# Kernel tuning notes

Hardware: AMD Instinct MI355X
Metric: run time of the kernel (lower is better)

The kernel has to match this reference:

```python
import jax, jax.numpy as jnp
import numpy as np

M, B, T, DIN, H, E, NEMB = 6, 128, 32, 64, 512, 512, 32


def setup_inputs() -> dict:
    key = jax.random.key(0)
    ks = jax.random.split(key, 6)
    return {
        "state_btD": jax.random.normal(ks[0], (B, T, M * DIN), dtype=jnp.float32),
        "emb_ids": jax.random.randint(ks[1], (B,), 0, NEMB),
        # stacked per-modality, per-embodiment adapter params (all modalities share dims)
        "W1": 0.02 * jax.random.normal(ks[2], (M, NEMB, DIN, H), dtype=jnp.float32),
        "b1": jnp.zeros((M, NEMB, H), dtype=jnp.float32),
        "W2": 0.02 * jax.random.normal(ks[3], (M, NEMB, H, E), dtype=jnp.float32),
        "b2": jnp.zeros((M, NEMB, E), dtype=jnp.float32),
        "type_embed": 0.02 * jax.random.normal(ks[4], (M, E), dtype=jnp.float32),
    }


def reference(state_btD, emb_ids, W1, b1, W2, b2, type_embed):
    Bb, Tt, _ = state_btD.shape
    # slices are contiguous equal-size chunks -> (B, T, M, DIN)
    x = state_btD.reshape(Bb, Tt, M, DIN)
    # layer1: per-sample gathered weights W1[:, emb_ids] -> (M, B, DIN, H)
    h = jax.nn.relu(
        jnp.einsum('btmi,mbih->btmh', x, W1[:, emb_ids])
        + b1[:, emb_ids].transpose(1, 0, 2)[:, None]  # (B,1,M,H)
    )
    # layer2 + type embed
    z = (
        jnp.einsum('btmh,mbho->btmo', h, W2[:, emb_ids])
        + b2[:, emb_ids].transpose(1, 0, 2)[:, None]
        + type_embed[None, None]  # (1,1,M,E)
    )
    # torch.cat(tokens, dim=1): modality-major along the token axis -> (B, M*T, E)
    return z.transpose(0, 2, 1, 3).reshape(Bb, M * Tt, E)
```

## Files before the change

kernel.cpp:

```cpp
#include <hip/hip_runtime.h>

#define MM   6
#define BB   128
#define TT   32
#define DIN  64
#define HH   512
#define EE   512
#define NEMB 32
#define XP   72
#define HP   520

typedef __attribute__((ext_vector_type(8))) short bf16x8;
typedef __attribute__((ext_vector_type(4))) float f32x4;

static __device__ __forceinline__ unsigned short f2bf(float f) {
    unsigned int u = __float_as_uint(f);
    u += 0x7FFFu + ((u >> 16) & 1u);
    return (unsigned short)(u >> 16);
}
static __device__ __forceinline__ float bf2f(unsigned short h) {
    return __uint_as_float(((unsigned int)h) << 16);
}
static __device__ __forceinline__ unsigned short f2bf_t(float f) {
    return (unsigned short)(__float_as_uint(f) >> 16);
}

__global__ void order_k(const int* __restrict__ emb_ids, int* __restrict__ ent) {
    __shared__ int cnt_s[NEMB], psum_s[NEMB], slot_s[BB], id_s[BB];
    int t = threadIdx.x;
    if (t < NEMB) cnt_s[t] = 0;
    __syncthreads();
    if (t < BB) { int id = emb_ids[t]; id_s[t] = id; slot_s[t] = atomicAdd(&cnt_s[id], 1); }
    __syncthreads();
    if (t == 0) { int r = 0; for (int i = 0; i < NEMB; ++i) { psum_s[i] = r; r += cnt_s[i]; } }
    __syncthreads();
    if (t < BB) {
        int id = id_s[t], sl = slot_s[t], base = psum_s[id] * MM, c = cnt_s[id];
        for (int mm = 0; mm < MM; ++mm) ent[base + mm * c + sl] = (t << 3) | mm;
    }
}

__global__ __launch_bounds__(512, 4) void tok_mfma5(
    const float* __restrict__ state,
    const int*   __restrict__ ent,
    const float* __restrict__ W1,
    const float* __restrict__ b1,
    const float* __restrict__ W2,
    const float* __restrict__ b2,
    const float* __restrict__ te,
    const int*   __restrict__ emb_ids,
    float* __restrict__ out)
{
    __shared__ __align__(16) unsigned short x_hi[TT][XP];
    __shared__ __align__(16) unsigned short x_lo[TT][XP];
    __shared__ __align__(16) unsigned short h_hi[TT][HP];
    __shared__ __align__(16) unsigned short h_lo[TT][HP];

    const int bid = blockIdx.x;
    const int s   = (bid & 7) * 96 + (bid >> 3);
    const int e   = ent[s];
    const int b   = e >> 3;
    const int m   = e & 7;
    const int id  = emb_ids[b];

    const int tid  = threadIdx.x;
    const int lane = tid & 63;
    const int w    = tid >> 6;
    const int lr   = lane & 15;
    const int lg   = lane >> 4;

    const float* W1p = W1 + (size_t)(m * NEMB + id) * DIN * HH;
    const float* b1p = b1 + (size_t)(m * NEMB + id) * HH;
    const float* W2p = W2 + (size_t)(m * NEMB + id) * HH * EE;
    const float* b2p = b2 + (size_t)(m * NEMB + id) * EE;
    const float* tep = te + m * EE;
    const float* xg  = state + (size_t)b * TT * (MM * DIN) + m * DIN;

    {
        int t  = tid >> 4;
        int i4 = tid & 15;
        float4 v = *reinterpret_cast<const float4*>(xg + (size_t)t * (MM * DIN) + i4 * 4);
        ushort4 hi, lo;
        hi.x = f2bf(v.x); lo.x = f2bf_t(v.x - bf2f(hi.x));
        hi.y = f2bf(v.y); lo.y = f2bf_t(v.y - bf2f(hi.y));
        hi.z = f2bf(v.z); lo.z = f2bf_t(v.z - bf2f(hi.z));
        hi.w = f2bf(v.w); lo.w = f2bf_t(v.w - bf2f(hi.w));
        *reinterpret_cast<ushort4*>(&x_hi[t][i4 * 4]) = hi;
        *reinterpret_cast<ushort4*>(&x_lo[t][i4 * 4]) = lo;
    }
    __syncthreads();

    bf16x8 xa_h[2][2], xa_l[2][2];
    #pragma unroll
    for (int rt = 0; rt < 2; ++rt)
        #pragma unroll
        for (int kk = 0; kk < 2; ++kk) {
            xa_h[rt][kk] = *reinterpret_cast<const bf16x8*>(&x_hi[rt * 16 + lr][kk * 32 + lg * 8]);
            xa_l[rt][kk] = *reinterpret_cast<const bf16x8*>(&x_lo[rt * 16 + lr][kk * 32 + lg * 8]);
        }

    #pragma unroll
    for (int j = 0; j < 4; ++j) {
        const int n = w * 64 + j * 16 + lr;
        float bv = b1p[n];
        f32x4 a0 = {bv, bv, bv, bv};
        f32x4 a1 = {bv, bv, bv, bv};
        #pragma unroll
        for (int kk = 0; kk < 2; ++kk) {
            const float* wp = W1p + (size_t)(kk * 32 + lg * 8) * HH + n;
            bf16x8 bh, bl;
            #pragma unroll
            for (int i = 0; i < 8; ++i) {
                float wv = wp[(size_t)i * HH];
                unsigned short h_ = f2bf(wv);
                bh[i] = (short)h_;
                bl[i] = (short)f2bf_t(wv - bf2f(h_));
            }
            a0 = __builtin_amdgcn_mfma_f32_16x16x32_bf16(xa_h[0][kk], bh, a0, 0, 0, 0);
            a0 = __builtin_amdgcn_mfma_f32_16x16x32_bf16(xa_h[0][kk], bl, a0, 0, 0, 0);
            a0 = __builtin_amdgcn_mfma_f32_16x16x32_bf16(xa_l[0][kk], bh, a0, 0, 0, 0);
            a1 = __builtin_amdgcn_mfma_f32_16x16x32_bf16(xa_h[1][kk], bh, a1, 0, 0, 0);
            a1 = __builtin_amdgcn_mfma_f32_16x16x32_bf16(xa_h[1][kk], bl, a1, 0, 0, 0);
            a1 = __builtin_amdgcn_mfma_f32_16x16x32_bf16(xa_l[1][kk], bh, a1, 0, 0, 0);
        }
        #pragma unroll
        for (int r = 0; r < 4; ++r) {
            float h0 = fmaxf(a0[r], 0.0f);
            unsigned short hh0 = f2bf(h0);
            h_hi[lg * 4 + r][n] = hh0;
            h_lo[lg * 4 + r][n] = f2bf_t(h0 - bf2f(hh0));
            float h1 = fmaxf(a1[r], 0.0f);
            unsigned short hh1 = f2bf(h1);
            h_hi[16 + lg * 4 + r][n] = hh1;
            h_lo[16 + lg * 4 + r][n] = f2bf_t(h1 - bf2f(hh1));
        }
    }
    __syncthreads();

    float bias2[4];
    #pragma unroll
    for (int j = 0; j < 4; ++j) {
        int n = w * 64 + j * 16 + lr;
        bias2[j] = b2p[n] + tep[n];
    }
    f32x4 acc[2][4];
    #pragma unroll
    for (int rt = 0; rt < 2; ++rt)
        #pragma unroll
        for (int j = 0; j < 4; ++j) {
            f32x4 t0 = {bias2[j], bias2[j], bias2[j], bias2[j]};
            acc[rt][j] = t0;
        }

    float cur[8];
    #pragma unroll
    for (int i = 0; i < 8; ++i)
        cur[i] = W2p[(size_t)(lg * 8 + i) * EE + (w * 64 + lr)];

    for (int kk = 0; kk < 16; ++kk) {
        bf16x8 ah0 = *reinterpret_cast<const bf16x8*>(&h_hi[lr][kk * 32 + lg * 8]);
        bf16x8 al0 = *reinterpret_cast<const bf16x8*>(&h_lo[lr][kk * 32 + lg * 8]);
        bf16x8 ah1 = *reinterpret_cast<const bf16x8*>(&h_hi[16 + lr][kk * 32 + lg * 8]);
        bf16x8 al1 = *reinterpret_cast<const bf16x8*>(&h_lo[16 + lr][kk * 32 + lg * 8]);
        #pragma unroll
        for (int j = 0; j < 4; ++j) {
            int nkk = (j == 3) ? kk + 1 : kk;
            int nj  = (j == 3) ? 0 : j + 1;
            float nxt[8];
            if (nkk < 16) {
                const float* wp = W2p + (size_t)(nkk * 32 + lg * 8) * EE + (w * 64 + nj * 16 + lr);
                #pragma unroll
                for (int i = 0; i < 8; ++i) nxt[i] = wp[(size_t)i * EE];
            } else {
                #pragma unroll
                for (int i = 0; i < 8; ++i) nxt[i] = 0.0f;
            }
            bf16x8 bh, bl;
            #pragma unroll
            for (int i = 0; i < 8; ++i) {
                unsigned short hb = f2bf(cur[i]);
                bh[i] = (short)hb;
                bl[i] = (short)f2bf_t(cur[i] - bf2f(hb));
            }
            acc[0][j] = __builtin_amdgcn_mfma_f32_16x16x32_bf16(ah0, bh, acc[0][j], 0, 0, 0);
            acc[0][j] = __builtin_amdgcn_mfma_f32_16x16x32_bf16(ah0, bl, acc[0][j], 0, 0, 0);
            acc[0][j] = __builtin_amdgcn_mfma_f32_16x16x32_bf16(al0, bh, acc[0][j], 0, 0, 0);
            acc[1][j] = __builtin_amdgcn_mfma_f32_16x16x32_bf16(ah1, bh, acc[1][j], 0, 0, 0);
            acc[1][j] = __builtin_amdgcn_mfma_f32_16x16x32_bf16(ah1, bl, acc[1][j], 0, 0, 0);
            acc[1][j] = __builtin_amdgcn_mfma_f32_16x16x32_bf16(al1, bh, acc[1][j], 0, 0, 0);
            #pragma unroll
            for (int i = 0; i < 8; ++i) cur[i] = nxt[i];
        }
    }

    float* outp = out + ((size_t)(b * MM + m) * TT) * EE;
    #pragma unroll
    for (int rt = 0; rt < 2; ++rt)
        #pragma unroll
        for (int j = 0; j < 4; ++j) {
            int n = w * 64 + j * 16 + lr;
            #pragma unroll
            for (int r = 0; r < 4; ++r) {
                int row = rt * 16 + lg * 4 + r;
                outp[(size_t)row * EE + n] = acc[rt][j][r];
            }
        }
}

extern "C" void kernel_launch(void* const* d_in, const int* in_sizes, int n_in,
                              void* d_out, int out_size, void* d_ws, size_t ws_size,
                              hipStream_t stream) {
    const float* state   = (const float*)d_in[0];
    const int*   emb_ids = (const int*)d_in[1];
    const float* W1      = (const float*)d_in[2];
    const float* b1      = (const float*)d_in[3];
    const float* W2      = (const float*)d_in[4];
    const float* b2      = (const float*)d_in[5];
    const float* te      = (const float*)d_in[6];
    float*       out     = (float*)d_out;

    int* ent = (int*)d_ws;

    order_k<<<dim3(1), dim3(128), 0, stream>>>(emb_ids, ent);
    tok_mfma5<<<dim3(BB * MM), dim3(512), 0, stream>>>(
        state, ent, W1, b1, W2, b2, te, emb_ids, out);
}
```

Measured before the change: 387.0 us.

## Stage W2 through LDS as pre-split bf16 pairs with 1024-thread blocks

Doubles the block to 1024 threads (16 waves, each covering 32 output columns) and stages W2 in 32-row chunks. Each chunk is loaded with coalesced float4 reads, split once into hi/lo bf16 pairs, and packed into shared memory, with the next chunk prefetched into registers. This replaces strided per-lane scalar global loads and repeated per-wave conversion with one conversion per element and LDS reads. It adds about 64KB of LDS per block, two barriers per k-step, and puts pressure on occupancy and registers under launch_bounds(1024,4).

```diff
diff --git a/kernel.cpp b/kernel.cpp
--- a/kernel.cpp
+++ b/kernel.cpp
@@ -9,6 +9,7 @@
 #define NEMB 32
 #define XP   72
 #define HP   520
+#define WS   514
 
 typedef __attribute__((ext_vector_type(8))) short bf16x8;
 typedef __attribute__((ext_vector_type(4))) float f32x4;
@@ -24,6 +25,11 @@
 static __device__ __forceinline__ unsigned short f2bf_t(float f) {
     return (unsigned short)(__float_as_uint(f) >> 16);
 }
+static __device__ __forceinline__ unsigned int packsplit(float v) {
+    unsigned short hi = f2bf(v);
+    unsigned short lo = f2bf_t(v - bf2f(hi));
+    return (unsigned int)hi | ((unsigned int)lo << 16);
+}
 
 __global__ void order_k(const int* __restrict__ emb_ids, int* __restrict__ ent) {
     __shared__ int cnt_s[NEMB], psum_s[NEMB], slot_s[BB], id_s[BB];
@@ -40,7 +46,7 @@
     }
 }
 
-__global__ __launch_bounds__(512, 4) void tok_mfma5(
+__global__ __launch_bounds__(1024, 4) void tok_mfma6(
     const float* __restrict__ state,
     const int*   __restrict__ ent,
     const float* __restrict__ W1,
@@ -55,10 +61,11 @@
     __shared__ __align__(16) unsigned short x_lo[TT][XP];
     __shared__ __align__(16) unsigned short h_hi[TT][HP];
     __shared__ __align__(16) unsigned short h_lo[TT][HP];
+    __shared__ __align__(16) unsigned int  w2t[32 * WS];
 
     const int bid = blockIdx.x;
-    const int s   = (bid & 7) * 96 + (bid >> 3);
-    const int e   = ent[s];
+    const int s0  = (bid & 7) * 96 + (bid >> 3);
+    const int e   = ent[s0];
     const int b   = e >> 3;
     const int m   = e & 7;
     const int id  = emb_ids[b];
@@ -76,7 +83,15 @@
     const float* tep = te + m * EE;
     const float* xg  = state + (size_t)b * TT * (MM * DIN) + m * DIN;
 
-    {
+    const int srow = tid >> 7;
+    const int scol = (tid & 127) * 4;
+    const float* wsrc = W2p + (size_t)srow * EE + scol;
+    float4 pa0 = *reinterpret_cast<const float4*>(wsrc);
+    float4 pa1 = *reinterpret_cast<const float4*>(wsrc + (size_t)8 * EE);
+    float4 pa2 = *reinterpret_cast<const float4*>(wsrc + (size_t)16 * EE);
+    float4 pa3 = *reinterpret_cast<const float4*>(wsrc + (size_t)24 * EE);
+
+    if (tid < 512) {
         int t  = tid >> 4;
         int i4 = tid & 15;
         float4 v = *reinterpret_cast<const float4*>(xg + (size_t)t * (MM * DIN) + i4 * 4);
@@ -100,8 +115,8 @@
         }
 
     #pragma unroll
-    for (int j = 0; j < 4; ++j) {
-        const int n = w * 64 + j * 16 + lr;
+    for (int j2 = 0; j2 < 2; ++j2) {
+        const int n = w * 32 + j2 * 16 + lr;
         float bv = b1p[n];
         f32x4 a0 = {bv, bv, bv, bv};
         f32x4 a1 = {bv, bv, bv, bv};
@@ -135,74 +150,83 @@
             h_lo[16 + lg * 4 + r][n] = f2bf_t(h1 - bf2f(hh1));
         }
     }
-    __syncthreads();
-
-    float bias2[4];
-    #pragma unroll
-    for (int j = 0; j < 4; ++j) {
-        int n = w * 64 + j * 16 + lr;
-        bias2[j] = b2p[n] + tep[n];
-    }
-    f32x4 acc[2][4];
+
+    float bias2[2];
+    #pragma unroll
+    for (int j2 = 0; j2 < 2; ++j2) {
+        int n = w * 32 + j2 * 16 + lr;
+        bias2[j2] = b2p[n] + tep[n];
+    }
+    f32x4 acc[2][2];
     #pragma unroll
     for (int rt = 0; rt < 2; ++rt)
         #pragma unroll
-        for (int j = 0; j < 4; ++j) {
-            f32x4 t0 = {bias2[j], bias2[j], bias2[j], bias2[j]};
-            acc[rt][j] = t0;
-        }
-
-    float cur[8];
-    #pragma unroll
-    for (int i = 0; i < 8; ++i)
-        cur[i] = W2p[(size_t)(lg * 8 + i) * EE + (w * 64 + lr)];
-
-    for (int kk = 0; kk < 16; ++kk) {
-        bf16x8 ah0 = *reinterpret_cast<const bf16x8*>(&h_hi[lr][kk * 32 + lg * 8]);
-        bf16x8 al0 = *reinterpret_cast<const bf16x8*>(&h_lo[lr][kk * 32 + lg * 8]);
-        bf16x8 ah1 = *reinterpret_cast<const bf16x8*>(&h_hi[16 + lr][kk * 32 + lg * 8]);
-        bf16x8 al1 = *reinterpret_cast<const bf16x8*>(&h_lo[16 + lr][kk * 32 + lg * 8]);
-        #pragma unroll
-        for (int j = 0; j < 4; ++j) {
-            int nkk = (j == 3) ? kk + 1 : kk;
-            int nj  = (j == 3) ? 0 : j + 1;
-            float nxt[8];
-            if (nkk < 16) {
-                const float* wp = W2p + (size_t)(nkk * 32 + lg * 8) * EE + (w * 64 + nj * 16 + lr);
-                #pragma unroll
-                for (int i = 0; i < 8; ++i) nxt[i] = wp[(size_t)i * EE];
-            } else {
-                #pragma unroll
-                for (int i = 0; i < 8; ++i) nxt[i] = 0.0f;
-            }
+        for (int j2 = 0; j2 < 2; ++j2) {
+            f32x4 t0 = {bias2[j2], bias2[j2], bias2[j2], bias2[j2]};
+            acc[rt][j2] = t0;
+        }
+    __syncthreads();
+
+    for (int s = 0; s < 16; ++s) {
+        {
+            unsigned int* wr0 = &w2t[(0 * 8 + srow) * WS + scol];
+            wr0[0] = packsplit(pa0.x); wr0[1] = packsplit(pa0.y);
+            wr0[2] = packsplit(pa0.z); wr0[3] = packsplit(pa0.w);
+            unsigned int* wr1 = &w2t[(1 * 8 + srow) * WS + scol];
+            wr1[0] = packsplit(pa1.x); wr1[1] = packsplit(pa1.y);
+            wr1[2] = packsplit(pa1.z); wr1[3] = packsplit(pa1.w);
+            unsigned int* wr2 = &w2t[(2 * 8 + srow) * WS + scol];
+            wr2[0] = packsplit(pa2.x); wr2[1] = packsplit(pa2.y);
+            wr2[2] = packsplit(pa2.z); wr2[3] = packsplit(pa2.w);
+            unsigned int* wr3 = &w2t[(3 * 8 + srow) * WS + scol];
+            wr3[0] = packsplit(pa3.x); wr3[1] = packsplit(pa3.y);
+            wr3[2] = packsplit(pa3.z); wr3[3] = packsplit(pa3.w);
+        }
+        __syncthreads();
+
+        if (s < 15) {
+            const float* nsrc = W2p + (size_t)((s + 1) * 32 + srow) * EE + scol;
+            pa0 = *reinterpret_cast<const float4*>(nsrc);
+            pa1 = *reinterpret_cast<const float4*>(nsrc + (size_t)8 * EE);
+            pa2 = *reinterpret_cast<const float4*>(nsrc + (size_t)16 * EE);
+            pa3 = *reinterpret_cast<const float4*>(nsrc + (size_t)24 * EE);
+        }
+
+        bf16x8 ah0 = *reinterpret_cast<const bf16x8*>(&h_hi[lr][s * 32 + lg * 8]);
+        bf16x8 al0 = *reinterpret_cast<const bf16x8*>(&h_lo[lr][s * 32 + lg * 8]);
+        bf16x8 ah1 = *reinterpret_cast<const bf16x8*>(&h_hi[16 + lr][s * 32 + lg * 8]);
+        bf16x8 al1 = *reinterpret_cast<const bf16x8*>(&h_lo[16 + lr][s * 32 + lg * 8]);
+
+        #pragma unroll
+        for (int j2 = 0; j2 < 2; ++j2) {
+            const int n = w * 32 + j2 * 16 + lr;
             bf16x8 bh, bl;
             #pragma unroll
             for (int i = 0; i < 8; ++i) {
-                unsigned short hb = f2bf(cur[i]);
-                bh[i] = (short)hb;
-                bl[i] = (short)f2bf_t(cur[i] - bf2f(hb));
+                unsigned int u = w2t[(lg * 8 + i) * WS + n];
+                bh[i] = (short)(u & 0xFFFFu);
+                bl[i] = (short)(u >> 16);
             }
-            acc[0][j] = __builtin_amdgcn_mfma_f32_16x16x32_bf16(ah0, bh, acc[0][j], 0, 0, 0);
-            acc[0][j] = __builtin_amdgcn_mfma_f32_16x16x32_bf16(ah0, bl, acc[0][j], 0, 0, 0);
-            acc[0][j] = __builtin_amdgcn_mfma_f32_16x16x32_bf16(al0, bh, acc[0][j], 0, 0, 0);
-            acc[1][j] = __builtin_amdgcn_mfma_f32_16x16x32_bf16(ah1, bh, acc[1][j], 0, 0, 0);
-            acc[1][j] = __builtin_amdgcn_mfma_f32_16x16x32_bf16(ah1, bl, acc[1][j], 0, 0, 0);
-            acc[1][j] = __builtin_amdgcn_mfma_f32_16x16x32_bf16(al1, bh, acc[1][j], 0, 0, 0);
-            #pragma unroll
-            for (int i = 0; i < 8; ++i) cur[i] = nxt[i];
-        }
+            acc[0][j2] = __builtin_amdgcn_mfma_f32_16x16x32_bf16(ah0, bh, acc[0][j2], 0, 0, 0);
+            acc[0][j2] = __builtin_amdgcn_mfma_f32_16x16x32_bf16(ah0, bl, acc[0][j2], 0, 0, 0);
+            acc[0][j2] = __builtin_amdgcn_mfma_f32_16x16x32_bf16(al0, bh, acc[0][j2], 0, 0, 0);
+            acc[1][j2] = __builtin_amdgcn_mfma_f32_16x16x32_bf16(ah1, bh, acc[1][j2], 0, 0, 0);
+            acc[1][j2] = __builtin_amdgcn_mfma_f32_16x16x32_bf16(ah1, bl, acc[1][j2], 0, 0, 0);
+            acc[1][j2] = __builtin_amdgcn_mfma_f32_16x16x32_bf16(al1, bh, acc[1][j2], 0, 0, 0);
+        }
+        __syncthreads();
     }
 
     float* outp = out + ((size_t)(b * MM + m) * TT) * EE;
     #pragma unroll
     for (int rt = 0; rt < 2; ++rt)
         #pragma unroll
-        for (int j = 0; j < 4; ++j) {
-            int n = w * 64 + j * 16 + lr;
+        for (int j2 = 0; j2 < 2; ++j2) {
+            int n = w * 32 + j2 * 16 + lr;
             #pragma unroll
             for (int r = 0; r < 4; ++r) {
                 int row = rt * 16 + lg * 4 + r;
-                outp[(size_t)row * EE + n] = acc[rt][j][r];
+                outp[(size_t)row * EE + n] = acc[rt][j2][r];
             }
         }
 }
@@ -222,6 +246,6 @@
     int* ent = (int*)d_ws;
 
     order_k<<<dim3(1), dim3(128), 0, stream>>>(emb_ids, ent);
-    tok_mfma5<<<dim3(BB * MM), dim3(512), 0, stream>>>(
+    tok_mfma6<<<dim3(BB * MM), dim3(1024), 0, stream>>>(
         state, ent, W1, b1, W2, b2, te, emb_ids, out);
 }
```

After: 374.1 us. -3.3%, faster.
